# Kernel tuning notes

Hardware: AMD Instinct MI355X
Metric: run time of the kernel (lower is better)

## Reference

```python
import jax, jax.numpy as jnp
import numpy as np

B, U, HEADS, S = 16, 1024, 8, 1024


def setup_inputs() -> dict:
    key = jax.random.key(0)
    k1, k2, k3, k4 = jax.random.split(key, 4)
    x = jax.random.normal(k1, (B, U, S), dtype=jnp.float32)
    mask = jax.random.randint(k2, (B, S, S), 0, 2).astype(bool)
    w_qkv = jax.random.normal(k3, (3 * U, U), dtype=jnp.float32) * 0.02
    w_out = jax.random.normal(k4, (U, U), dtype=jnp.float32) * 0.02
    return {"x": x, "mask": mask, "w_qkv": w_qkv, "w_out": w_out}


def reference(x, mask, w_qkv, w_out):
    # x: (B, U, S), mask: (B, n_queries, n_keys) bool
    b, u, s = x.shape
    h = HEADS
    c = u // h  # head (chunk) size
    scale = 1.0 / np.sqrt(c).astype(np.float32)

    # 1x1-conv QKV projection (bias=False): (3U, U) x (B, U, S) -> (B, 3U, S)
    qkv = jnp.einsum('ou,bus->bos', w_qkv, x)
    Q, K, V = jnp.split(qkv, 3, axis=1)           # each (B, U, S)
    Qh = Q.reshape(b, h, c, s)
    Kh = K.reshape(b, h, c, s)
    Vh = V.reshape(b, h, c, s)

    # attention logits: (B, H, n_q, n_k)
    A = jnp.einsum('bhcq,bhck->bhqk', Qh, Kh)

    # relu activation with per-query valid-key-count normalization
    m = mask.sum(axis=2)[:, :, None]              # (B, n_q, 1) count of valid keys
    n_elem = jnp.where(mask, m, 1).astype(A.dtype)[:, None]  # (B, 1, n_q, n_k)
    mask_b = mask[:, None]                        # broadcast over heads
    A = jnp.where(mask_b, jax.nn.relu(A) * scale, -jnp.inf)
    A = A / n_elem
    A = jnp.where(jnp.isinf(A), jnp.zeros((), A.dtype), A)

    # attention-value aggregation (faithful math of broadcast+sum): (B, H, C, n_q)
    Ch = jnp.einsum('bhqk,bhck->bhcq', A, Vh)
    Cc = Ch.reshape(b, u, s)

    # finishing 1x1-conv linear layer
    return jnp.einsum('ou,bus->bos', w_out, Cc)
```

## Files before the change

kernel.cpp:

```cpp
#include <hip/hip_runtime.h>

#define B_DIM 16
#define U_DIM 1024
#define H_DIM 8
#define S_DIM 1024
#define C_DIM 128
#define KD 1024
#define SCALE 0.08838834764831845f

typedef __attribute__((ext_vector_type(8))) short s16x8;
typedef __attribute__((ext_vector_type(4))) float f32x4;

__device__ __forceinline__ void gll16(const void* g, void* l) {
  __builtin_amdgcn_global_load_lds(
      (const __attribute__((address_space(1))) unsigned int*)g,
      (__attribute__((address_space(3))) unsigned int*)l, 16, 0, 0);
}
__device__ __forceinline__ unsigned short f2bf(float f) {
  unsigned u = __float_as_uint(f);
  u += 0x7FFF + ((u >> 16) & 1u);
  return (unsigned short)(u >> 16);
}
#define MFMA16(a, b, c) __builtin_amdgcn_mfma_f32_16x16x32_bf16(a, b, c, 0, 0, 0)

__global__ void detect_mask(const unsigned char* __restrict__ mask_raw, int* __restrict__ flag) {
  __shared__ int not01, notf;
  if (threadIdx.x == 0) { not01 = 0; notf = 0; }
  __syncthreads();
  const unsigned int* p = (const unsigned int*)mask_raw;
  int l01 = 0, lf = 0;
  for (int i = threadIdx.x; i < 4096; i += 256) {
    unsigned int v = p[i];
    if (v != 0u && v != 1u) l01 = 1;
    if (v != 0u && v != 0x3F800000u) lf = 1;
  }
  if (l01) atomicOr(&not01, 1);
  if (lf) atomicOr(&notf, 1);
  __syncthreads();
  if (threadIdx.x == 0) flag[0] = (!not01) ? 0 : ((!notf) ? 2 : 1);
}

__global__ __launch_bounds__(256) void pack_mask(const unsigned char* __restrict__ mask_raw,
                                                 const int* __restrict__ flag,
                                                 unsigned long long* __restrict__ bits) {
  __shared__ unsigned char tile[64][80];
  const int t = threadIdx.x;
  const int kt = blockIdx.x * 64, qw = blockIdx.y, b = blockIdx.z;
  const int mk = flag[0];
  const int q = t >> 2, kbase = (t & 3) * 16;
  const size_t row = (size_t)(b * S_DIM + qw * 64 + q);
  if (mk == 1) {
    uint4 v = *(const uint4*)(mask_raw + (row << 10) + kt + kbase);
    *(uint4*)&tile[q][kbase] = v;
  } else if (mk == 0) {
    const int* p = (const int*)mask_raw + (row << 10) + kt + kbase;
#pragma unroll
    for (int j = 0; j < 4; ++j) {
      int4 v = ((const int4*)p)[j];
      uchar4 o;
      o.x = v.x ? 1 : 0; o.y = v.y ? 1 : 0; o.z = v.z ? 1 : 0; o.w = v.w ? 1 : 0;
      *(uchar4*)&tile[q][kbase + j * 4] = o;
    }
  } else {
    const float* p = (const float*)mask_raw + (row << 10) + kt + kbase;
#pragma unroll
    for (int j = 0; j < 4; ++j) {
      float4 v = ((const float4*)p)[j];
      uchar4 o;
      o.x = (v.x != 0.f) ? 1 : 0; o.y = (v.y != 0.f) ? 1 : 0;
      o.z = (v.z != 0.f) ? 1 : 0; o.w = (v.w != 0.f) ? 1 : 0;
      *(uchar4*)&tile[q][kbase + j * 4] = o;
    }
  }
  __syncthreads();
  const int wave = t >> 6, lane = t & 63;
#pragma unroll
  for (int qq = 0; qq < 16; ++qq) {
    int qr = wave * 16 + qq;
    unsigned long long bal = __ballot(tile[qr][lane] != 0);
    if (lane == 0)
      bits[(size_t)blockIdx.x * (B_DIM * S_DIM) + (size_t)b * S_DIM + qw * 64 + qr] = bal;
  }
}

__global__ __launch_bounds__(256) void invm_from_bits(const unsigned long long* __restrict__ bits,
                                                      float* __restrict__ invm) {
  int idx = blockIdx.x * 256 + threadIdx.x;
  int s = 0;
#pragma unroll
  for (int kt = 0; kt < S_DIM / 64; ++kt)
    s += __popcll(bits[(size_t)kt * (B_DIM * S_DIM) + idx]);
  invm[idx] = (s > 0) ? (SCALE / (float)s) : 0.f;
}

__global__ __launch_bounds__(256) void cvt_bf16(const float* __restrict__ in,
                                                unsigned short* __restrict__ out, int n) {
  int i = (blockIdx.x * 256 + threadIdx.x) * 4;
  if (i < n) {
    float4 v = *(const float4*)(in + i);
    ushort4 o;
    o.x = f2bf(v.x); o.y = f2bf(v.y); o.z = f2bf(v.z); o.w = f2bf(v.w);
    *(ushort4*)(out + i) = o;
  }
}

__global__ __launch_bounds__(256) void transpose_x(const float* __restrict__ x,
                                                   unsigned short* __restrict__ xT) {
  __shared__ float T[32][33];
  const int t = threadIdx.x, r = t >> 3, c4 = (t & 7) * 4;
  const int s0 = blockIdx.x * 32, u0 = blockIdx.y * 32;
  const size_t base = (size_t)blockIdx.z * U_DIM * S_DIM;
  float4 v = *(const float4*)(x + base + (size_t)(u0 + r) * S_DIM + s0 + c4);
  T[r][c4 + 0] = v.x; T[r][c4 + 1] = v.y; T[r][c4 + 2] = v.z; T[r][c4 + 3] = v.w;
  __syncthreads();
  ushort4 o;
  o.x = f2bf(T[c4 + 0][r]); o.y = f2bf(T[c4 + 1][r]);
  o.z = f2bf(T[c4 + 2][r]); o.w = f2bf(T[c4 + 3][r]);
  *(ushort4*)(xT + base + (size_t)(s0 + r) * U_DIM + u0 + c4) = o;
}

__global__ __launch_bounds__(256) void transpose_v(const unsigned short* __restrict__ qkvT,
                                                   unsigned short* __restrict__ VT) {
  __shared__ unsigned short T[32][34];
  const int t = threadIdx.x, r = t >> 3, c4 = (t & 7) * 4;
  const int k0 = blockIdx.x * 32, c0 = blockIdx.y * 32;
  const unsigned short* qb = qkvT + (size_t)blockIdx.z * S_DIM * (3 * U_DIM);
  ushort4 v = *(const ushort4*)(qb + (size_t)(k0 + r) * (3 * U_DIM) + 2 * U_DIM + c0 + c4);
  T[r][c4 + 0] = v.x; T[r][c4 + 1] = v.y; T[r][c4 + 2] = v.z; T[r][c4 + 3] = v.w;
  __syncthreads();
  ushort4 o;
  o.x = T[c4 + 0][r]; o.y = T[c4 + 1][r]; o.z = T[c4 + 2][r]; o.w = T[c4 + 3][r];
  *(ushort4*)(VT + (size_t)blockIdx.z * U_DIM * S_DIM + (size_t)(c0 + r) * S_DIM + k0 + c4) = o;
}

template <typename OUT>
__global__ __launch_bounds__(256) void gemm_tt(const unsigned short* __restrict__ A,
                                               const unsigned short* __restrict__ Bm,
                                               OUT* __restrict__ D,
                                               long long sAb, long long sBb, long long sDb,
                                               int N) {
  __shared__ unsigned short sA[128 * 64];
  __shared__ unsigned short sB[128 * 64];
  const int tid = threadIdx.x, wave = tid >> 6, lane = tid & 63;
  const int l15 = lane & 15, quad = lane >> 4;
  const int m0 = blockIdx.y * 128, n0 = blockIdx.x * 128;
  A += (size_t)blockIdx.z * sAb;
  Bm += (size_t)blockIdx.z * sBb;
  D += (size_t)blockIdx.z * sDb;
  const int wm = (wave >> 1) * 64, wn = (wave & 1) * 64;
  f32x4 acc[4][4] = {};

  for (int k0 = 0; k0 < KD; k0 += 64) {
#pragma unroll
    for (int t = 0; t < 4; ++t) {
      int p = wave * 256 + t * 64 + lane;
      int row = p >> 3, kc = (p & 7) ^ (row & 7);
      gll16(A + (size_t)(m0 + row) * KD + k0 + kc * 8, &sA[(wave * 256 + t * 64) * 8]);
    }
#pragma unroll
    for (int t = 0; t < 4; ++t) {
      int p = wave * 256 + t * 64 + lane;
      int row = p >> 3, kc = (p & 7) ^ (row & 7);
      gll16(Bm + (size_t)(n0 + row) * KD + k0 + kc * 8, &sB[(wave * 256 + t * 64) * 8]);
    }
    __syncthreads();
#pragma unroll
    for (int kk = 0; kk < 2; ++kk) {
      s16x8 af[4], bf[4];
#pragma unroll
      for (int i = 0; i < 4; ++i) {
        int row = wm + i * 16 + l15;
        af[i] = *(const s16x8*)&sA[row * 64 + ((kk * 4 + quad) ^ (row & 7)) * 8];
      }
#pragma unroll
      for (int j = 0; j < 4; ++j) {
        int row = wn + j * 16 + l15;
        bf[j] = *(const s16x8*)&sB[row * 64 + ((kk * 4 + quad) ^ (row & 7)) * 8];
      }
#pragma unroll
      for (int i = 0; i < 4; ++i)
#pragma unroll
        for (int j = 0; j < 4; ++j) acc[i][j] = MFMA16(af[i], bf[j], acc[i][j]);
    }
    __syncthreads();
  }
#pragma unroll
  for (int i = 0; i < 4; ++i)
#pragma unroll
    for (int j = 0; j < 4; ++j) {
      f32x4 v = acc[i][j];
#pragma unroll
      for (int r = 0; r < 4; ++r) {
        int m = m0 + wm + i * 16 + quad * 4 + r;
        int n = n0 + wn + j * 16 + l15;
        if constexpr (sizeof(OUT) == 2) D[(size_t)m * N + n] = f2bf(v[r]);
        else D[(size_t)m * N + n] = v[r];
      }
    }
}

__global__ __launch_bounds__(256, 2) void attn_mfma(const unsigned short* __restrict__ qkvT,
                                                    const unsigned short* __restrict__ VT,
                                                    const unsigned long long* __restrict__ bits,
                                                    const float* __restrict__ invm,
                                                    unsigned short* __restrict__ CcT, int b0) {
  __shared__ unsigned short QV[64 * 128];
  __shared__ unsigned short Ks[64 * 128];
  __shared__ unsigned short Vs[128 * 64];
  __shared__ unsigned short Ps[64 * 64];
  __shared__ float invs[64];

  const int tid = threadIdx.x, wave = tid >> 6, lane = tid & 63;
  const int l15 = lane & 15, quad = lane >> 4;
  const int qt = blockIdx.x, h = blockIdx.y, z = blockIdx.z;
  const int q0 = qt * 64, b = b0 + z;
  const unsigned short* qB = qkvT + (size_t)z * S_DIM * (3 * U_DIM);
  const unsigned short* Vb = VT + (size_t)z * U_DIM * S_DIM + (size_t)h * C_DIM * S_DIM;

#pragma unroll
  for (int t = 0; t < 4; ++t) {
    int p = wave * 256 + t * 64 + lane;
    int row = p >> 4, c = (p & 15) ^ (row & 7);
    gll16(qB + (size_t)(q0 + row) * (3 * U_DIM) + h * C_DIM + c * 8,
          &QV[(wave * 256 + t * 64) * 8]);
    gll16(qB + (size_t)(row) * (3 * U_DIM) + U_DIM + h * C_DIM + c * 8,
          &Ks[(wave * 256 + t * 64) * 8]);
    int vrow = p >> 3, vkc = (p & 7) ^ (vrow & 7);
    gll16(Vb + (size_t)vrow * S_DIM + vkc * 8, &Vs[(wave * 256 + t * 64) * 8]);
  }
  if (tid < 64) invs[tid] = invm[(size_t)b * S_DIM + q0 + tid];
  __syncthreads();

  s16x8 qf[4][4];
#pragma unroll
  for (int j = 0; j < 4; ++j)
#pragma unroll
    for (int kk = 0; kk < 4; ++kk) {
      int row = j * 16 + l15;
      qf[j][kk] = *(const s16x8*)&QV[row * 128 + ((kk * 4 + quad) ^ (row & 7)) * 8];
    }
  float invf[4];
#pragma unroll
  for (int j = 0; j < 4; ++j) invf[j] = invs[j * 16 + l15];

  f32x4 pacc[4][2] = {};

  for (int kt = 0; kt < S_DIM / 64; ++kt) {
    unsigned long long w64[4];
    {
      const unsigned long long* mw =
          bits + (size_t)kt * (B_DIM * S_DIM) + (size_t)b * S_DIM + q0;
#pragma unroll
      for (int j = 0; j < 4; ++j) w64[j] = mw[j * 16 + l15];
    }

    s16x8 af[4];
#pragma unroll
    for (int kk = 0; kk < 4; ++kk) {
      int row = wave * 16 + l15;
      af[kk] = *(const s16x8*)&Ks[row * 128 + ((kk * 4 + quad) ^ (row & 7)) * 8];
    }
    f32x4 sacc[4] = {};
#pragma unroll
    for (int kk = 0; kk < 4; ++kk)
#pragma unroll
      for (int j = 0; j < 4; ++j) sacc[j] = MFMA16(af[kk], qf[j][kk], sacc[j]);

#pragma unroll
    for (int j = 0; j < 4; ++j) {
      unsigned int pk[2];
#pragma unroll
      for (int half = 0; half < 2; ++half) {
        unsigned int w = 0;
#pragma unroll
        for (int r2 = 0; r2 < 2; ++r2) {
          int r = half * 2 + r2;
          float p = fmaxf(sacc[j][r], 0.f) * invf[j];
          p = ((w64[j] >> (wave * 16 + quad * 4 + r)) & 1ull) ? p : 0.f;
          w |= (unsigned int)f2bf(p) << (r2 * 16);
        }
        pk[half] = w;
      }
      int q = j * 16 + l15;
      int chunk = (wave * 2 + (quad >> 1)) ^ (q & 7);
      *(uint2*)&Ps[q * 64 + chunk * 8 + (quad & 1) * 4] = make_uint2(pk[0], pk[1]);
    }
    __syncthreads();

    if (kt < S_DIM / 64 - 1) {
      const int kn = (kt + 1) * 64;
      unsigned short* vdst = (kt & 1) ? Vs : QV;
#pragma unroll
      for (int t = 0; t < 4; ++t) {
        int p = wave * 256 + t * 64 + lane;
        int row = p >> 4, c = (p & 15) ^ (row & 7);
        gll16(qB + (size_t)(kn + row) * (3 * U_DIM) + U_DIM + h * C_DIM + c * 8,
              &Ks[(wave * 256 + t * 64) * 8]);
        int vrow = p >> 3, vkc = (p & 7) ^ (vrow & 7);
        gll16(Vb + (size_t)vrow * S_DIM + kn + vkc * 8, &vdst[(wave * 256 + t * 64) * 8]);
      }
    }

    const unsigned short* vbuf = (kt & 1) ? QV : Vs;
#pragma unroll
    for (int ks = 0; ks < 2; ++ks) {
      s16x8 pf[4], vf[2];
#pragma unroll
      for (int i = 0; i < 4; ++i) {
        int row = i * 16 + l15;
        pf[i] = *(const s16x8*)&Ps[row * 64 + ((ks * 4 + quad) ^ (row & 7)) * 8];
      }
#pragma unroll
      for (int j = 0; j < 2; ++j) {
        int row = wave * 32 + j * 16 + l15;
        vf[j] = *(const s16x8*)&vbuf[row * 64 + ((ks * 4 + quad) ^ (row & 7)) * 8];
      }
#pragma unroll
      for (int i = 0; i < 4; ++i)
#pragma unroll
        for (int j = 0; j < 2; ++j) pacc[i][j] = MFMA16(pf[i], vf[j], pacc[i][j]);
    }
    __syncthreads();
  }

  unsigned short* cb = CcT + (size_t)z * S_DIM * U_DIM;
#pragma unroll
  for (int i = 0; i < 4; ++i)
#pragma unroll
    for (int j = 0; j < 2; ++j) {
      f32x4 v = pacc[i][j];
#pragma unroll
      for (int r = 0; r < 4; ++r) {
        int q = q0 + i * 16 + quad * 4 + r;
        int c = h * C_DIM + wave * 32 + j * 16 + l15;
        cb[(size_t)q * U_DIM + c] = f2bf(v[r]);
      }
    }
}

extern "C" void kernel_launch(void* const* d_in, const int* in_sizes, int n_in,
                              void* d_out, int out_size, void* d_ws, size_t ws_size,
                              hipStream_t stream) {
  const float* x = (const float*)d_in[0];
  const unsigned char* mask_raw = (const unsigned char*)d_in[1];
  const float* w_qkv = (const float*)d_in[2];
  const float* w_out = (const float*)d_in[3];
  float* out = (float*)d_out;

  char* ws = (char*)d_ws;
  int* flag = (int*)ws;
  float* invm = (float*)(ws + 256);
  unsigned long long* bits = (unsigned long long*)(ws + 256 + 65536);
  unsigned short* wqkv_bf = (unsigned short*)((char*)bits + (size_t)B_DIM * S_DIM * 16 * 8);
  unsigned short* wout_bf = (unsigned short*)((char*)wqkv_bf + (size_t)3 * U_DIM * U_DIM * 2);
  char* heap = (char*)wout_bf + (size_t)U_DIM * U_DIM * 2;

  const size_t xT_pb = (size_t)U_DIM * S_DIM * 2;
  const size_t qkvT_pb = (size_t)3 * U_DIM * S_DIM * 2;
  const size_t vT_pb = (size_t)U_DIM * S_DIM * 2;
  const size_t ccT_pb = (size_t)U_DIM * S_DIM * 2;
  const size_t per_batch = xT_pb + qkvT_pb + vT_pb + ccT_pb;
  const size_t fixed = (size_t)(heap - ws);
  int nb = (ws_size > fixed) ? (int)((ws_size - fixed) / per_batch) : 1;
  if (nb < 1) nb = 1;
  if (nb > B_DIM) nb = B_DIM;

  unsigned short* xT = (unsigned short*)heap;
  unsigned short* qkvT = (unsigned short*)(heap + (size_t)nb * xT_pb);
  unsigned short* VT = (unsigned short*)(heap + (size_t)nb * (xT_pb + qkvT_pb));
  unsigned short* CcT = (unsigned short*)(heap + (size_t)nb * (xT_pb + qkvT_pb + vT_pb));

  detect_mask<<<1, 256, 0, stream>>>(mask_raw, flag);
  pack_mask<<<dim3(S_DIM / 64, S_DIM / 64, B_DIM), 256, 0, stream>>>(mask_raw, flag, bits);
  invm_from_bits<<<(B_DIM * S_DIM) / 256, 256, 0, stream>>>(bits, invm);
  cvt_bf16<<<(3 * U_DIM * U_DIM) / 1024, 256, 0, stream>>>(w_qkv, wqkv_bf, 3 * U_DIM * U_DIM);
  cvt_bf16<<<(U_DIM * U_DIM) / 1024, 256, 0, stream>>>(w_out, wout_bf, U_DIM * U_DIM);

  for (int b0 = 0; b0 < B_DIM; b0 += nb) {
    int cnt = (B_DIM - b0 < nb) ? (B_DIM - b0) : nb;
    transpose_x<<<dim3(S_DIM / 32, U_DIM / 32, cnt), 256, 0, stream>>>(
        x + (size_t)b0 * U_DIM * S_DIM, xT);
    gemm_tt<unsigned short><<<dim3(3 * U_DIM / 128, S_DIM / 128, cnt), 256, 0, stream>>>(
        xT, wqkv_bf, qkvT, (long long)U_DIM * S_DIM, 0LL, (long long)3 * U_DIM * S_DIM, 3 * U_DIM);
    transpose_v<<<dim3(S_DIM / 32, U_DIM / 32, cnt), 256, 0, stream>>>(qkvT, VT);
    attn_mfma<<<dim3(S_DIM / 64, H_DIM, cnt), 256, 0, stream>>>(
        qkvT, VT, bits, invm, CcT, b0);
    gemm_tt<float><<<dim3(S_DIM / 128, U_DIM / 128, cnt), 256, 0, stream>>>(
        wout_bf, CcT, out + (size_t)b0 * U_DIM * S_DIM, 0LL,
        (long long)U_DIM * S_DIM, (long long)U_DIM * S_DIM, S_DIM);
  }
}
```

Baseline: 480.7 us.

## Remap workgroups across XCDs, raise MFMA priority, use packed bf16 convert

Both the GEMM and attention kernels now remap the linear workgroup id so that consecutive logical tiles land on the same XCD, which should improve L2 reuse of shared Q/K/V and weight tiles. The attention kernel wraps its MFMA loops in s_setprio so waves issuing matrix ops get scheduling priority. It also replaces the manual round-to-nearest bf16 packing with the hardware v_cvt_pk_bf16_f32 instruction and extracts the mask bits once per j. The remap assumes the grid size divides evenly by 8, and the attention remap hardcodes 16x8 for the x and y grid dimensions.

```diff
diff --git a/kernel.cpp b/kernel.cpp
--- a/kernel.cpp
+++ b/kernel.cpp
@@ -143,10 +143,17 @@
   __shared__ unsigned short sB[128 * 64];
   const int tid = threadIdx.x, wave = tid >> 6, lane = tid & 63;
   const int l15 = lane & 15, quad = lane >> 4;
-  const int m0 = blockIdx.y * 128, n0 = blockIdx.x * 128;
-  A += (size_t)blockIdx.z * sAb;
-  Bm += (size_t)blockIdx.z * sBb;
-  D += (size_t)blockIdx.z * sDb;
+  const unsigned int Lb = blockIdx.x + gridDim.x * (blockIdx.y + gridDim.y * blockIdx.z);
+  const unsigned int nwg = gridDim.x * gridDim.y * gridDim.z;
+  const unsigned int logical = (Lb & 7u) * (nwg >> 3) + (Lb >> 3);
+  const int bx = logical % gridDim.x;
+  const unsigned int rem = logical / gridDim.x;
+  const int by = rem % gridDim.y;
+  const int bz = rem / gridDim.y;
+  const int m0 = by * 128, n0 = bx * 128;
+  A += (size_t)bz * sAb;
+  Bm += (size_t)bz * sBb;
+  D += (size_t)bz * sDb;
   const int wm = (wave >> 1) * 64, wn = (wave & 1) * 64;
   f32x4 acc[4][4] = {};
 
@@ -212,7 +219,10 @@
 
   const int tid = threadIdx.x, wave = tid >> 6, lane = tid & 63;
   const int l15 = lane & 15, quad = lane >> 4;
-  const int qt = blockIdx.x, h = blockIdx.y, z = blockIdx.z;
+  const int L = blockIdx.x + 16 * (blockIdx.y + 8 * blockIdx.z);
+  const int cpx = (16 * H_DIM * gridDim.z) >> 3;
+  const int logical = (L & 7) * cpx + (L >> 3);
+  const int qt = logical & 15, h = (logical >> 4) & 7, z = logical >> 7;
   const int q0 = qt * 64, b = b0 + z;
   const unsigned short* qB = qkvT + (size_t)z * S_DIM * (3 * U_DIM);
   const unsigned short* Vb = VT + (size_t)z * U_DIM * S_DIM + (size_t)h * C_DIM * S_DIM;
@@ -261,29 +271,28 @@
       af[kk] = *(const s16x8*)&Ks[row * 128 + ((kk * 4 + quad) ^ (row & 7)) * 8];
     }
     f32x4 sacc[4] = {};
+    __builtin_amdgcn_s_setprio(1);
 #pragma unroll
     for (int kk = 0; kk < 4; ++kk)
 #pragma unroll
       for (int j = 0; j < 4; ++j) sacc[j] = MFMA16(af[kk], qf[j][kk], sacc[j]);
+    __builtin_amdgcn_s_setprio(0);
 
 #pragma unroll
     for (int j = 0; j < 4; ++j) {
-      unsigned int pk[2];
-#pragma unroll
-      for (int half = 0; half < 2; ++half) {
-        unsigned int w = 0;
-#pragma unroll
-        for (int r2 = 0; r2 < 2; ++r2) {
-          int r = half * 2 + r2;
-          float p = fmaxf(sacc[j][r], 0.f) * invf[j];
-          p = ((w64[j] >> (wave * 16 + quad * 4 + r)) & 1ull) ? p : 0.f;
-          w |= (unsigned int)f2bf(p) << (r2 * 16);
-        }
-        pk[half] = w;
-      }
+      const unsigned int m4 = (unsigned int)(w64[j] >> (wave * 16 + quad * 4)) & 0xFu;
+      float p[4];
+#pragma unroll
+      for (int r = 0; r < 4; ++r) {
+        float t = fmaxf(sacc[j][r], 0.f) * invf[j];
+        p[r] = ((m4 >> r) & 1u) ? t : 0.f;
+      }
+      unsigned int pk0, pk1;
+      asm("v_cvt_pk_bf16_f32 %0, %1, %2" : "=v"(pk0) : "v"(p[0]), "v"(p[1]));
+      asm("v_cvt_pk_bf16_f32 %0, %1, %2" : "=v"(pk1) : "v"(p[2]), "v"(p[3]));
       int q = j * 16 + l15;
       int chunk = (wave * 2 + (quad >> 1)) ^ (q & 7);
-      *(uint2*)&Ps[q * 64 + chunk * 8 + (quad & 1) * 4] = make_uint2(pk[0], pk[1]);
+      *(uint2*)&Ps[q * 64 + chunk * 8 + (quad & 1) * 4] = make_uint2(pk0, pk1);
     }
     __syncthreads();
 
@@ -315,10 +324,12 @@
         int row = wave * 32 + j * 16 + l15;
         vf[j] = *(const s16x8*)&vbuf[row * 64 + ((ks * 4 + quad) ^ (row & 7)) * 8];
       }
+      __builtin_amdgcn_s_setprio(1);
 #pragma unroll
       for (int i = 0; i < 4; ++i)
 #pragma unroll
         for (int j = 0; j < 2; ++j) pacc[i][j] = MFMA16(pf[i], vf[j], pacc[i][j]);
+      __builtin_amdgcn_s_setprio(0);
     }
     __syncthreads();
   }
```

After: 484.7 us. About the same (+0.9%).
